# Performance work log

Hardware: AMD Instinct MI355X
Metric: run time of the kernel (lower is better)

The kernel has to match this reference:

```python
import jax, jax.numpy as jnp
import numpy as np

B, S, D, H, DFF, L, VOCAB = 4, 2048, 512, 8, 2048, 6, 32000
DK = D // H


def positional_encoding(n_step, d):
    pos = jnp.arange(n_step, dtype=jnp.float32)[:, None]            # (S,1)
    i = jnp.arange(d, dtype=jnp.float32)                            # (D,)
    ang = pos * (1.0 / jnp.power(10000.0, 2.0 * jnp.floor(i / 2.0) / d))
    odd = (jnp.arange(d) % 2).astype(bool)
    return jnp.where(odd, jnp.cos(ang), jnp.sin(ang))               # (S,D)


def layer_norm(x, g, b, eps=1e-6):
    m = x.mean(-1, keepdims=True)
    v = ((x - m) ** 2).mean(-1, keepdims=True)
    return g * (x - m) * jax.lax.rsqrt(v + eps) + b


def mha(Q, K, V, Wq, bq, Wo, bo, mask):
    # Faithful to source: Wq is (buggily) used for Q, K and V projections.
    def split(t):
        return t.reshape(t.shape[0], -1, H, DK).transpose(0, 2, 1, 3)  # (B,H,S,dk)
    q = split(Q @ Wq + bq)
    k = split(K @ Wq + bq)
    v = split(V @ Wq + bq)
    scores = jnp.einsum('bhqd,bhkd->bhqk', q, k) / jnp.sqrt(jnp.float32(DK))
    if mask is not None:
        scores = scores + mask * (-1e9)
    attn = jax.nn.softmax(scores, axis=-1)
    out = jnp.einsum('bhqk,bhkd->bhqd', attn, v)
    out = out.transpose(0, 2, 1, 3).reshape(Q.shape[0], -1, D)
    return out @ Wo + bo


def setup_inputs() -> dict:
    key = jax.random.key(0)
    ks = jax.random.split(key, 16)
    inputs = jax.random.randint(ks[0], (B, S), 0, VOCAB)
    enc_inputs = jax.random.normal(ks[1], (B, S, D), dtype=jnp.float32)
    # causal mask (1 = masked) broadcast over heads, per source mask*-1e9 convention
    comb = 1.0 - jnp.tril(jnp.ones((S, S), dtype=jnp.float32))
    comb_mask = jnp.broadcast_to(comb, (B, 1, S, S))
    padding_mask = jnp.zeros((B, 1, 1, S), dtype=jnp.float32)
    s = 0.02
    emb = jax.random.normal(ks[2], (VOCAB, D), dtype=jnp.float32) * s
    Wq1 = jax.random.normal(ks[3], (L, D, D), dtype=jnp.float32) * s
    bq1 = jnp.zeros((L, D), dtype=jnp.float32)
    Wo1 = jax.random.normal(ks[4], (L, D, D), dtype=jnp.float32) * s
    bo1 = jnp.zeros((L, D), dtype=jnp.float32)
    Wq2 = jax.random.normal(ks[5], (L, D, D), dtype=jnp.float32) * s
    bq2 = jnp.zeros((L, D), dtype=jnp.float32)
    Wo2 = jax.random.normal(ks[6], (L, D, D), dtype=jnp.float32) * s
    bo2 = jnp.zeros((L, D), dtype=jnp.float32)
    W1 = jax.random.normal(ks[7], (L, D, DFF), dtype=jnp.float32) * s
    b1 = jnp.zeros((L, DFF), dtype=jnp.float32)
    W2 = jax.random.normal(ks[8], (L, DFF, D), dtype=jnp.float32) * s
    b2 = jnp.zeros((L, D), dtype=jnp.float32)
    ln_g = jnp.ones((L, 3, D), dtype=jnp.float32)
    ln_b = jnp.zeros((L, 3, D), dtype=jnp.float32)
    return dict(inputs=inputs, enc_inputs=enc_inputs, comb_mask=comb_mask,
                padding_mask=padding_mask, emb=emb, Wq1=Wq1, bq1=bq1, Wo1=Wo1,
                bo1=bo1, Wq2=Wq2, bq2=bq2, Wo2=Wo2, bo2=bo2, W1=W1, b1=b1,
                W2=W2, b2=b2, ln_g=ln_g, ln_b=ln_b)


def reference(inputs, enc_inputs, comb_mask, padding_mask, emb, Wq1, bq1, Wo1,
              bo1, Wq2, bq2, Wo2, bo2, W1, b1, W2, b2, ln_g, ln_b):
    # embedding + sinusoidal positional encoding (dropout = identity at eval)
    x = emb[inputs] * jnp.sqrt(jnp.float32(D)) + positional_encoding(S, D)
    for l in range(L):
        a1 = mha(x, x, x, Wq1[l], bq1[l], Wo1[l], bo1[l], comb_mask)
        x1 = layer_norm(a1 + x, ln_g[l, 0], ln_b[l, 0])
        a2 = mha(x1, enc_inputs, enc_inputs, Wq2[l], bq2[l], Wo2[l], bo2[l], padding_mask)
        x2 = layer_norm(a2 + x1, ln_g[l, 1], ln_b[l, 1])
        f = jax.nn.relu(x2 @ W1[l] + b1[l]) @ W2[l] + b2[l]
        x = layer_norm(x2 + f, ln_g[l, 2], ln_b[l, 2])
    return x
```

## Files before the change

### kernel.cpp

```cpp
#include <hip/hip_runtime.h>
#include <hip/hip_bf16.h>
#include <cstddef>
#include <cstdint>

#define BB   4
#define SS   2048
#define DD   512
#define HH   8
#define DFFC 2048
#define LLC  6
#define DKH  64
#define MMR  (BB * SS)

typedef short s16x8 __attribute__((ext_vector_type(8)));
typedef short s16x4 __attribute__((ext_vector_type(4)));
typedef float f32x4 __attribute__((ext_vector_type(4)));
typedef unsigned short us4 __attribute__((ext_vector_type(4)));
typedef unsigned int u32;
typedef unsigned int u32x4 __attribute__((ext_vector_type(4)));

__device__ __forceinline__ unsigned short f2bf(float f) {
  union { float f; unsigned int u; } v; v.f = f;
  const unsigned int u = v.u;
  return (unsigned short)((u + 0x7FFFu + ((u >> 16) & 1u)) >> 16);
}
__device__ __forceinline__ float bflo(u32 u) { return __uint_as_float(u << 16); }
__device__ __forceinline__ float bfhi(u32 u) { return __uint_as_float(u & 0xffff0000u); }

__device__ __forceinline__ s16x8 ld8(const unsigned short* p) {
  return *(const s16x8*)p;
}

__device__ __forceinline__ u32 cvtpk(float a, float b) {
  u32 r;
  asm("v_cvt_pk_bf16_f32 %0, %1, %2" : "=v"(r) : "v"(a), "v"(b));
  return r;
}

__device__ __forceinline__ void gload16(const unsigned short* g, unsigned short* l) {
  __builtin_amdgcn_global_load_lds(
      (const __attribute__((address_space(1))) void*)g,
      (__attribute__((address_space(3))) void*)l, 16, 0, 0);
}

__global__ __launch_bounds__(256) void k_embed_pe(const int* __restrict__ toks,
                                                  const float* __restrict__ emb,
                                                  unsigned short* __restrict__ xb) {
  const int t = blockIdx.x;
  const int s = t & (SS - 1);
  const int tok = toks[t];
  const float ln10k = 9.210340371976184f;
  for (int d = threadIdx.x; d < DD; d += 256) {
    const int e = d >> 1;
    const float ex = 2.0f * (float)e * (1.0f / (float)DD);
    const float freq = expf(-ex * ln10k);
    const float ang = (float)s * freq;
    const float pe = (d & 1) ? cosf(ang) : sinf(ang);
    const float v = emb[(size_t)tok * DD + d] * 22.62741699796952f + pe;
    xb[(size_t)t * DD + d] = f2bf(v);
  }
}

__global__ __launch_bounds__(256) void k_f32_to_bf16(const float* __restrict__ src,
                                                     unsigned short* __restrict__ dst) {
  const int i = (blockIdx.x * 256 + threadIdx.x) * 4;
  const float4 v = *(const float4*)(src + i);
  us4 w;
  w.x = f2bf(v.x); w.y = f2bf(v.y); w.z = f2bf(v.z); w.w = f2bf(v.w);
  *(us4*)(dst + i) = w;
}

__global__ __launch_bounds__(256) void k_wt(const float* s0, const float* s1,
                                            const float* s2, const float* s3,
                                            const float* s4, const float* s5,
                                            unsigned short* d0, unsigned short* d1,
                                            unsigned short* d2, unsigned short* d3,
                                            unsigned short* d4, unsigned short* d5) {
  const int t = blockIdx.x;
  const int tid = threadIdx.x;
  const float* src; unsigned short* dst; int K, N, tile, lntn;
  if (t < 256) {
    const int m = t >> 6; tile = t & 63; K = 512; N = 512; lntn = 3;
    src = (m == 0) ? s0 : (m == 1) ? s1 : (m == 2) ? s2 : s3;
    dst = (m == 0) ? d0 : (m == 1) ? d1 : (m == 2) ? d2 : d3;
  } else if (t < 512) {
    src = s4; dst = d4; K = 512; N = 2048; tile = t - 256; lntn = 5;
  } else {
    src = s5; dst = d5; K = 2048; N = 512; tile = t - 512; lntn = 3;
  }
  const int tn = tile & ((1 << lntn) - 1);
  const int tk = tile >> lntn;
  const int k0 = tk * 64, n0 = tn * 64;

  __shared__ unsigned short T[64][68];
#pragma unroll
  for (int i = 0; i < 4; ++i) {
    const int f = i * 256 + tid;
    const int r = f >> 4, c4 = (f & 15) << 2;
    const float4 v = *(const float4*)(src + (size_t)(k0 + r) * N + n0 + c4);
    us4 w;
    w.x = f2bf(v.x); w.y = f2bf(v.y); w.z = f2bf(v.z); w.w = f2bf(v.w);
    *(us4*)&T[r][c4] = w;
  }
  __syncthreads();
#pragma unroll
  for (int i = 0; i < 4; ++i) {
    const int f = i * 256 + tid;
    const int n = f >> 4, k4 = (f & 15) << 2;
    us4 w;
    w.x = T[k4 + 0][n]; w.y = T[k4 + 1][n];
    w.z = T[k4 + 2][n]; w.w = T[k4 + 3][n];
    *(us4*)&dst[(size_t)(n0 + n) * K + k0 + k4] = w;
  }
}

template<int BN, bool RELU, bool VT>
__global__ __launch_bounds__(256) void k_gemm_mfma(const unsigned short* __restrict__ A,
                                                   const unsigned short* __restrict__ Bt,
                                                   const float* __restrict__ bias,
                                                   unsigned short* __restrict__ Cb,
                                                   unsigned short* __restrict__ Vt,
                                                   int voff, int M, int N, int K) {
  constexpr int NT = BN / 32;
  __shared__ unsigned short As[128 * 64];
  __shared__ unsigned short Bs[BN * 64];

  const int tid = threadIdx.x;
  const int wave = tid >> 6, lane = tid & 63;
  const int quad = lane >> 4, l16 = lane & 15;
  const int wm = wave & 1, wn = wave >> 1;
  const int mbase = blockIdx.x * 128, nbase = blockIdx.y * BN;

  f32x4 acc[4][NT];
#pragma unroll
  for (int mt = 0; mt < 4; ++mt)
#pragma unroll
    for (int nt = 0; nt < NT; ++nt) acc[mt][nt] = (f32x4){0.f, 0.f, 0.f, 0.f};

  for (int kb = 0; kb < K; kb += 64) {
    __syncthreads();
#pragma unroll
    for (int i = 0; i < 4; ++i) {
      const int c = i * 256 + wave * 64 + lane;
      const int m = c >> 3;
      const int k8 = (c & 7) ^ (m & 7);
      gload16(A + (size_t)(mbase + m) * K + kb + k8 * 8,
              As + (size_t)(i * 256 + wave * 64) * 8);
    }
#pragma unroll
    for (int i = 0; i < BN / 32; ++i) {
      const int c = i * 256 + wave * 64 + lane;
      const int n = c >> 3;
      const int k8 = (c & 7) ^ (n & 7);
      gload16(Bt + (size_t)(nbase + n) * K + kb + k8 * 8,
              Bs + (size_t)(i * 256 + wave * 64) * 8);
    }
    __syncthreads();
#pragma unroll
    for (int kh = 0; kh < 2; ++kh) {
      s16x8 af[4];
#pragma unroll
      for (int mt = 0; mt < 4; ++mt) {
        const int m = wm * 64 + mt * 16 + l16;
        const int cc = m * 8 + ((kh * 4 + quad) ^ (m & 7));
        af[mt] = ld8(As + cc * 8);
      }
#pragma unroll
      for (int nt = 0; nt < NT; ++nt) {
        const int n = wn * (BN / 2) + nt * 16 + l16;
        const int cc = n * 8 + ((kh * 4 + quad) ^ (n & 7));
        const s16x8 bf = ld8(Bs + cc * 8);
#pragma unroll
        for (int mt = 0; mt < 4; ++mt)
          acc[mt][nt] = __builtin_amdgcn_mfma_f32_16x16x32_bf16(af[mt], bf, acc[mt][nt], 0, 0, 0);
      }
    }
  }

#pragma unroll
  for (int nt = 0; nt < NT; ++nt) {
    const int col = nbase + wn * (BN / 2) + nt * 16 + l16;
    const float bv = bias[col];
#pragma unroll
    for (int mt = 0; mt < 4; ++mt) {
      const int row0 = mbase + wm * 64 + mt * 16 + quad * 4;
      float vv[4];
#pragma unroll
      for (int r = 0; r < 4; ++r) {
        float v = acc[mt][nt][r] + bv;
        if (RELU) v = fmaxf(v, 0.0f);
        vv[r] = v;
        Cb[(size_t)(row0 + r) * N + col] = f2bf(v);
      }
      if (VT) {
        if (row0 >= voff) {
          const int vrow = row0 - voff;
          const int bb = vrow >> 11, s0 = vrow & 2047;
          const int g = (s0 >> 2) & 15;
          const int pos = (g & 8) + ((g & 3) << 1) + ((g >> 2) & 1);
          const int s0p = (s0 & ~63) | (pos << 2);
          us4 o;
          o.x = f2bf(vv[0]); o.y = f2bf(vv[1]); o.z = f2bf(vv[2]); o.w = f2bf(vv[3]);
          *(us4*)(Vt + ((size_t)((bb * 8 + (col >> 6)) * 64 + (col & 63))) * SS + s0p) = o;
        }
      }
    }
  }
}

__global__ __launch_bounds__(512, 4) void k_attn_mfma(const unsigned short* __restrict__ Qp,
                                                      const unsigned short* __restrict__ Kp,
                                                      const unsigned short* __restrict__ Vtp,
                                                      unsigned short* __restrict__ Out,
                                                      int causal) {
  __shared__ __align__(16) unsigned char smem[34816];
  unsigned short* KsB = (unsigned short*)smem;
  unsigned short* VsB = (unsigned short*)(smem + 16384);

  const int hb = blockIdx.x;
  const int h = hb & 7, b = hb >> 3;
  const int by = blockIdx.y;
  const int qt = causal ? ((by < 8) ? (15 - by) : (by - 8)) : by;
  const int tid = threadIdx.x;
  const int w = tid >> 6, lane = tid & 63;
  const int quad = lane >> 4, l16 = lane & 15;
  const int qg = w & 3, ks = w >> 2;

  s16x8 aq[2][2];
#pragma unroll
  for (int mt = 0; mt < 2; ++mt) {
    const int qrow = b * SS + qt * 128 + qg * 32 + mt * 16 + l16;
#pragma unroll
    for (int kh = 0; kh < 2; ++kh) {
      s16x8 v = *(const s16x8*)(Qp + (size_t)qrow * DD + h * DKH + kh * 32 + quad * 8);
#pragma unroll
      for (int j = 0; j < 8; ++j) {
        const unsigned int u = ((unsigned int)(unsigned short)v[j]) << 16;
        const float f = __uint_as_float(u) * 0.125f;
        v[j] = (short)(unsigned short)(__float_as_uint(f) >> 16);
      }
      aq[mt][kh] = v;
    }
  }

  f32x4 O[2][4];
  float l_r[2];
#pragma unroll
  for (int mt = 0; mt < 2; ++mt) {
    l_r[mt] = 0.f;
#pragma unroll
    for (int i = 0; i < 4; ++i) O[mt][i] = (f32x4){0.f, 0.f, 0.f, 0.f};
  }

  const unsigned short* Kb = Kp + (size_t)(b * SS) * DD + h * DKH;
  const unsigned short* Vb = Vtp + (size_t)hb * DKH * SS;

  const int nkt = causal ? (2 * qt + 2) : (SS / 64);

  auto stage = [&](int kt2, int buf) {
    const int r = tid >> 3, c8 = tid & 7;
    gload16(Kb + (size_t)(kt2 * 64 + r) * DD + ((c8 ^ (r & 7)) << 3),
            KsB + buf * 4096 + w * 512);
    gload16(Vb + (size_t)r * SS + kt2 * 64 + ((c8 ^ (r & 7)) << 3),
            VsB + buf * 4096 + w * 512);
  };

  stage(0, 0);
  for (int kt = 0; kt < nkt; ++kt) {
    __syncthreads();
    if (kt + 1 < nkt) stage(kt + 1, (kt + 1) & 1);
    const unsigned short* ksp = KsB + (kt & 1) * 4096;
    const unsigned short* vsp = VsB + (kt & 1) * 4096;

    s16x8 kf[2][2];
#pragma unroll
    for (int kg = 0; kg < 2; ++kg) {
      const int row = ks * 32 + kg * 16 + l16;
#pragma unroll
      for (int kh = 0; kh < 2; ++kh)
        kf[kg][kh] = ld8(ksp + (row * 8 + ((kh * 4 + quad) ^ (row & 7))) * 8);
    }

    f32x4 S[2][2];
    __builtin_amdgcn_s_setprio(1);
#pragma unroll
    for (int mt = 0; mt < 2; ++mt)
#pragma unroll
      for (int kg = 0; kg < 2; ++kg) {
        f32x4 s = (f32x4){0.f, 0.f, 0.f, 0.f};
        s = __builtin_amdgcn_mfma_f32_16x16x32_bf16(kf[kg][0], aq[mt][0], s, 0, 0, 0);
        s = __builtin_amdgcn_mfma_f32_16x16x32_bf16(kf[kg][1], aq[mt][1], s, 0, 0, 0);
        S[mt][kg] = s;
      }
    __builtin_amdgcn_s_setprio(0);

    s16x8 vbf[4];
#pragma unroll
    for (int nt = 0; nt < 4; ++nt) {
      const int d = nt * 16 + l16;
      vbf[nt] = ld8(vsp + (d * 8 + ((ks * 4 + quad) ^ (d & 7))) * 8);
    }

    s16x8 pa[2];
#pragma unroll
    for (int mt = 0; mt < 2; ++mt) {
      const int qb = qt * 128 + qg * 32 + mt * 16;
      const bool needmask = causal && (kt * 64 + 63 > qb);
      const int q = qb + l16;
      float pv[2][4];
#pragma unroll
      for (int kg = 0; kg < 2; ++kg) {
#pragma unroll
        for (int r = 0; r < 4; ++r) {
          float p = __expf(S[mt][kg][r]);
          if (needmask) {
            const int key = kt * 64 + ks * 32 + kg * 16 + quad * 4 + r;
            if (key > q) p = 0.0f;
          }
          pv[kg][r] = p;
        }
      }
      l_r[mt] += ((pv[0][0] + pv[0][1]) + (pv[0][2] + pv[0][3]))
               + ((pv[1][0] + pv[1][1]) + (pv[1][2] + pv[1][3]));
      u32x4 pk;
      pk.x = cvtpk(pv[0][0], pv[0][1]);
      pk.y = cvtpk(pv[0][2], pv[0][3]);
      pk.z = cvtpk(pv[1][0], pv[1][1]);
      pk.w = cvtpk(pv[1][2], pv[1][3]);
      pa[mt] = __builtin_bit_cast(s16x8, pk);
    }

    __builtin_amdgcn_s_setprio(1);
#pragma unroll
    for (int nt = 0; nt < 4; ++nt)
#pragma unroll
      for (int mt = 0; mt < 2; ++mt)
        O[mt][nt] = __builtin_amdgcn_mfma_f32_16x16x32_bf16(pa[mt], vbf[nt], O[mt][nt], 0, 0, 0);
    __builtin_amdgcn_s_setprio(0);
  }

  float lq[2][4];
#pragma unroll
  for (int mt = 0; mt < 2; ++mt) {
    float l = l_r[mt];
    l += __shfl_xor(l, 16);
    l += __shfl_xor(l, 32);
#pragma unroll
    for (int r = 0; r < 4; ++r)
      lq[mt][r] = __shfl(l, quad * 4 + r);
  }

  __syncthreads();
  float* Obuf = (float*)smem;
  float* Lbuf = (float*)(smem + 33792);
  if (ks == 1) {
#pragma unroll
    for (int mt = 0; mt < 2; ++mt)
#pragma unroll
      for (int r = 0; r < 4; ++r) {
        const int row = qg * 32 + mt * 16 + quad * 4 + r;
        if (l16 == 0) Lbuf[row] = lq[mt][r];
#pragma unroll
        for (int nt = 0; nt < 4; ++nt)
          Obuf[(size_t)row * 66 + nt * 16 + l16] = O[mt][nt][r];
      }
  }
  __syncthreads();
  if (ks == 0) {
#pragma unroll
    for (int mt = 0; mt < 2; ++mt)
#pragma unroll
      for (int r = 0; r < 4; ++r) {
        const int row = qg * 32 + mt * 16 + quad * 4 + r;
        const float linv = 1.0f / (lq[mt][r] + Lbuf[row]);
        unsigned short* orow = Out + (size_t)(b * SS + qt * 128 + row) * DD + h * DKH;
#pragma unroll
        for (int nt = 0; nt < 4; ++nt)
          orow[nt * 16 + l16] = f2bf((O[mt][nt][r] + Obuf[(size_t)row * 66 + nt * 16 + l16]) * linv);
      }
  }
}

__device__ __forceinline__ float block_reduce_sum(float v) {
  __shared__ float red[4];
#pragma unroll
  for (int off = 32; off > 0; off >>= 1) v += __shfl_down(v, off);
  const int lane = threadIdx.x & 63;
  const int w = threadIdx.x >> 6;
  __syncthreads();
  if (lane == 0) red[w] = v;
  __syncthreads();
  return red[0] + red[1] + red[2] + red[3];
}

template<bool F32OUT>
__global__ __launch_bounds__(256) void k_add_ln(const unsigned short* __restrict__ a,
                                                const unsigned short* __restrict__ r,
                                                const float* __restrict__ g,
                                                const float* __restrict__ be,
                                                unsigned short* __restrict__ ob,
                                                float* __restrict__ of) {
  const int row = blockIdx.x;
  const int t = threadIdx.x;
  const size_t base = (size_t)row * DD + t * 2;
  const u32 av = *(const u32*)(a + base);
  const u32 rv = *(const u32*)(r + base);
  const float v0 = bflo(av) + bflo(rv);
  const float v1 = bfhi(av) + bfhi(rv);
  const float s = block_reduce_sum(v0 + v1);
  const float mean = s * (1.0f / (float)DD);
  const float d0 = v0 - mean;
  const float d1 = v1 - mean;
  const float var = block_reduce_sum(d0 * d0 + d1 * d1) * (1.0f / (float)DD);
  const float inv = rsqrtf(var + 1e-6f);
  const float o0 = g[t * 2] * d0 * inv + be[t * 2];
  const float o1 = g[t * 2 + 1] * d1 * inv + be[t * 2 + 1];
  const u32 o = (u32)f2bf(o0) | ((u32)f2bf(o1) << 16);
  *(u32*)(ob + base) = o;
  if (F32OUT) {
    of[base]     = o0;
    of[base + 1] = o1;
  }
}

extern "C" void kernel_launch(void* const* d_in, const int* in_sizes, int n_in,
                              void* d_out, int out_size, void* d_ws, size_t ws_size,
                              hipStream_t stream) {
  const int*   toks = (const int*)d_in[0];
  const float* enc  = (const float*)d_in[1];
  const float* emb  = (const float*)d_in[4];
  const float* Wq1  = (const float*)d_in[5];
  const float* bq1  = (const float*)d_in[6];
  const float* Wo1  = (const float*)d_in[7];
  const float* bo1  = (const float*)d_in[8];
  const float* Wq2  = (const float*)d_in[9];
  const float* bq2  = (const float*)d_in[10];
  const float* Wo2  = (const float*)d_in[11];
  const float* bo2  = (const float*)d_in[12];
  const float* W1   = (const float*)d_in[13];
  const float* b1   = (const float*)d_in[14];
  const float* W2   = (const float*)d_in[15];
  const float* b2   = (const float*)d_in[16];
  const float* lng  = (const float*)d_in[17];
  const float* lnb  = (const float*)d_in[18];
  float* out = (float*)d_out;

  char* p = (char*)d_ws;
  unsigned short* Wq1t = (unsigned short*)p; p += (size_t)512 * 512 * 2;
  unsigned short* Wo1t = (unsigned short*)p; p += (size_t)512 * 512 * 2;
  unsigned short* Wq2t = (unsigned short*)p; p += (size_t)512 * 512 * 2;
  unsigned short* Wo2t = (unsigned short*)p; p += (size_t)512 * 512 * 2;
  unsigned short* W1t  = (unsigned short*)p; p += (size_t)2048 * 512 * 2;
  unsigned short* W2t  = (unsigned short*)p; p += (size_t)512 * 2048 * 2;
  unsigned short* Xcur = (unsigned short*)p; p += (size_t)MMR * DD * 2;
  unsigned short* Cat  = (unsigned short*)p; p += (size_t)2 * MMR * DD * 2;
  unsigned short* Pm   = (unsigned short*)p; p += (size_t)2 * MMR * DD * 2;
  unsigned short* Ab   = (unsigned short*)p; p += (size_t)MMR * DD * 2;
  unsigned short* Gb   = (unsigned short*)p; p += (size_t)MMR * DD * 2;
  unsigned short* X2b  = (unsigned short*)p; p += (size_t)MMR * DD * 2;
  unsigned short* Vt   = (unsigned short*)p; p += (size_t)MMR * DD * 2;
  unsigned short* Hb   = (unsigned short*)p; p += (size_t)MMR * DFFC * 2;
  unsigned short* encb = Cat + (size_t)MMR * DD;

  const dim3 blk(256);
  const dim3 blkA(512);
  const dim3 gP(MMR / 128, DD / 64);
  const dim3 gM(2 * MMR / 128, DD / 64);
  const dim3 gF1(MMR / 128, DFFC / 128);
  const dim3 gAttn(HH * BB, SS / 128);

  k_embed_pe<<<MMR, blk, 0, stream>>>(toks, emb, Xcur);
  k_f32_to_bf16<<<(MMR * DD) / 1024, blk, 0, stream>>>(enc, encb);

  for (int l = 0; l < LLC; ++l) {
    const float* wq1 = Wq1 + (size_t)l * DD * DD;
    const float* wo1 = Wo1 + (size_t)l * DD * DD;
    const float* wq2 = Wq2 + (size_t)l * DD * DD;
    const float* wo2 = Wo2 + (size_t)l * DD * DD;
    const float* w1  = W1  + (size_t)l * DD * DFFC;
    const float* w2  = W2  + (size_t)l * DFFC * DD;
    const float* bq1l = bq1 + (size_t)l * DD;
    const float* bo1l = bo1 + (size_t)l * DD;
    const float* bq2l = bq2 + (size_t)l * DD;
    const float* bo2l = bo2 + (size_t)l * DD;
    const float* b1l  = b1  + (size_t)l * DFFC;
    const float* b2l  = b2  + (size_t)l * DD;
    const float* g0 = lng + ((size_t)l * 3 + 0) * DD;
    const float* e0 = lnb + ((size_t)l * 3 + 0) * DD;
    const float* g1 = lng + ((size_t)l * 3 + 1) * DD;
    const float* e1 = lnb + ((size_t)l * 3 + 1) * DD;
    const float* g2 = lng + ((size_t)l * 3 + 2) * DD;
    const float* e2 = lnb + ((size_t)l * 3 + 2) * DD;

    k_wt<<<768, blk, 0, stream>>>(wq1, wo1, wq2, wo2, w1, w2,
                                  Wq1t, Wo1t, Wq2t, Wo2t, W1t, W2t);

    k_gemm_mfma<64, false, true><<<gP, blk, 0, stream>>>(Xcur, Wq1t, bq1l, Pm, Vt, 0, MMR, DD, DD);
    k_attn_mfma<<<gAttn, blkA, 0, stream>>>(Pm, Pm, Vt, Ab, 1);
    k_gemm_mfma<64, false, false><<<gP, blk, 0, stream>>>(Ab, Wo1t, bo1l, Gb, nullptr, 0, MMR, DD, DD);
    k_add_ln<false><<<MMR, blk, 0, stream>>>(Gb, Xcur, g0, e0, Cat, nullptr);

    k_gemm_mfma<64, false, true><<<gM, blk, 0, stream>>>(Cat, Wq2t, bq2l, Pm, Vt, MMR, 2 * MMR, DD, DD);
    k_attn_mfma<<<gAttn, blkA, 0, stream>>>(Pm, Pm + (size_t)MMR * DD, Vt, Ab, 0);
    k_gemm_mfma<64, false, false><<<gP, blk, 0, stream>>>(Ab, Wo2t, bo2l, Gb, nullptr, 0, MMR, DD, DD);
    k_add_ln<false><<<MMR, blk, 0, stream>>>(Gb, Cat, g1, e1, X2b, nullptr);

    k_gemm_mfma<128, true, false><<<gF1, blk, 0, stream>>>(X2b, W1t, b1l, Hb, nullptr, 0, MMR, DFFC, DD);
    k_gemm_mfma<64, false, false><<<gP, blk, 0, stream>>>(Hb, W2t, b2l, Gb, nullptr, 0, MMR, DD, DFFC);
    if (l == LLC - 1)
      k_add_ln<true><<<MMR, blk, 0, stream>>>(Gb, X2b, g2, e2, Xcur, out);
    else
      k_add_ln<false><<<MMR, blk, 0, stream>>>(Gb, X2b, g2, e2, Xcur, nullptr);
  }
}
```

Baseline: 1.532 ms.

## Double-buffer GEMM shared tiles and use one wave per row in add+layernorm

The GEMM kernel now keeps two shared-memory buffers for the A and B tiles and issues the next K-tile's async loads before computing on the current one. This overlaps global-to-LDS traffic with MFMA work, at the cost of twice the LDS per block and possibly lower occupancy. The add+layernorm kernel is rewritten so each 64-lane wave handles one row with 16-byte vector loads and stores and wave shuffle reductions. This removes the block-level reductions and their __syncthreads. The LN launch grid changes to four rows per block.

```diff
diff --git a/kernel.cpp b/kernel.cpp
--- a/kernel.cpp
+++ b/kernel.cpp
@@ -122,8 +122,8 @@
                                                    unsigned short* __restrict__ Vt,
                                                    int voff, int M, int N, int K) {
   constexpr int NT = BN / 32;
-  __shared__ unsigned short As[128 * 64];
-  __shared__ unsigned short Bs[BN * 64];
+  __shared__ unsigned short As[2][128 * 64];
+  __shared__ unsigned short Bs[2][BN * 64];
 
   const int tid = threadIdx.x;
   const int wave = tid >> 6, lane = tid & 63;
@@ -137,25 +137,32 @@
 #pragma unroll
     for (int nt = 0; nt < NT; ++nt) acc[mt][nt] = (f32x4){0.f, 0.f, 0.f, 0.f};
 
-  for (int kb = 0; kb < K; kb += 64) {
-    __syncthreads();
+  auto stage = [&](int kb, int buf) {
 #pragma unroll
     for (int i = 0; i < 4; ++i) {
       const int c = i * 256 + wave * 64 + lane;
       const int m = c >> 3;
       const int k8 = (c & 7) ^ (m & 7);
-      gload16(A + (size_t)(mbase + m) * K + kb + k8 * 8,
-              As + (size_t)(i * 256 + wave * 64) * 8);
+      gload16(A + (size_t)(mbase + m) * K + kb * 64 + k8 * 8,
+              As[buf] + (size_t)(i * 256 + wave * 64) * 8);
     }
 #pragma unroll
     for (int i = 0; i < BN / 32; ++i) {
       const int c = i * 256 + wave * 64 + lane;
       const int n = c >> 3;
       const int k8 = (c & 7) ^ (n & 7);
-      gload16(Bt + (size_t)(nbase + n) * K + kb + k8 * 8,
-              Bs + (size_t)(i * 256 + wave * 64) * 8);
-    }
+      gload16(Bt + (size_t)(nbase + n) * K + kb * 64 + k8 * 8,
+              Bs[buf] + (size_t)(i * 256 + wave * 64) * 8);
+    }
+  };
+
+  const int nkb = K / 64;
+  stage(0, 0);
+  for (int kb = 0; kb < nkb; ++kb) {
     __syncthreads();
+    if (kb + 1 < nkb) stage(kb + 1, (kb + 1) & 1);
+    const unsigned short* as = As[kb & 1];
+    const unsigned short* bs = Bs[kb & 1];
 #pragma unroll
     for (int kh = 0; kh < 2; ++kh) {
       s16x8 af[4];
@@ -163,13 +170,13 @@
       for (int mt = 0; mt < 4; ++mt) {
         const int m = wm * 64 + mt * 16 + l16;
         const int cc = m * 8 + ((kh * 4 + quad) ^ (m & 7));
-        af[mt] = ld8(As + cc * 8);
+        af[mt] = ld8(as + cc * 8);
       }
 #pragma unroll
       for (int nt = 0; nt < NT; ++nt) {
         const int n = wn * (BN / 2) + nt * 16 + l16;
         const int cc = n * 8 + ((kh * 4 + quad) ^ (n & 7));
-        const s16x8 bf = ld8(Bs + cc * 8);
+        const s16x8 bf = ld8(bs + cc * 8);
 #pragma unroll
         for (int mt = 0; mt < 4; ++mt)
           acc[mt][nt] = __builtin_amdgcn_mfma_f32_16x16x32_bf16(af[mt], bf, acc[mt][nt], 0, 0, 0);
@@ -381,18 +388,6 @@
   }
 }
 
-__device__ __forceinline__ float block_reduce_sum(float v) {
-  __shared__ float red[4];
-#pragma unroll
-  for (int off = 32; off > 0; off >>= 1) v += __shfl_down(v, off);
-  const int lane = threadIdx.x & 63;
-  const int w = threadIdx.x >> 6;
-  __syncthreads();
-  if (lane == 0) red[w] = v;
-  __syncthreads();
-  return red[0] + red[1] + red[2] + red[3];
-}
-
 template<bool F32OUT>
 __global__ __launch_bounds__(256) void k_add_ln(const unsigned short* __restrict__ a,
                                                 const unsigned short* __restrict__ r,
@@ -400,26 +395,50 @@
                                                 const float* __restrict__ be,
                                                 unsigned short* __restrict__ ob,
                                                 float* __restrict__ of) {
-  const int row = blockIdx.x;
-  const int t = threadIdx.x;
-  const size_t base = (size_t)row * DD + t * 2;
-  const u32 av = *(const u32*)(a + base);
-  const u32 rv = *(const u32*)(r + base);
-  const float v0 = bflo(av) + bflo(rv);
-  const float v1 = bfhi(av) + bfhi(rv);
-  const float s = block_reduce_sum(v0 + v1);
+  const int row = blockIdx.x * 4 + (threadIdx.x >> 6);
+  const int lane = threadIdx.x & 63;
+  const size_t base = (size_t)row * DD + lane * 8;
+  const u32x4 av = *(const u32x4*)(a + base);
+  const u32x4 rv = *(const u32x4*)(r + base);
+  float v[8];
+  float s = 0.f;
+#pragma unroll
+  for (int i = 0; i < 4; ++i) {
+    const float lo = bflo(av[i]) + bflo(rv[i]);
+    const float hi = bfhi(av[i]) + bfhi(rv[i]);
+    v[2 * i] = lo; v[2 * i + 1] = hi;
+    s += lo + hi;
+  }
+#pragma unroll
+  for (int off = 32; off > 0; off >>= 1) s += __shfl_xor(s, off);
   const float mean = s * (1.0f / (float)DD);
-  const float d0 = v0 - mean;
-  const float d1 = v1 - mean;
-  const float var = block_reduce_sum(d0 * d0 + d1 * d1) * (1.0f / (float)DD);
-  const float inv = rsqrtf(var + 1e-6f);
-  const float o0 = g[t * 2] * d0 * inv + be[t * 2];
-  const float o1 = g[t * 2 + 1] * d1 * inv + be[t * 2 + 1];
-  const u32 o = (u32)f2bf(o0) | ((u32)f2bf(o1) << 16);
-  *(u32*)(ob + base) = o;
+  float vs = 0.f;
+#pragma unroll
+  for (int i = 0; i < 8; ++i) { v[i] -= mean; vs += v[i] * v[i]; }
+#pragma unroll
+  for (int off = 32; off > 0; off >>= 1) vs += __shfl_xor(vs, off);
+  const float inv = rsqrtf(vs * (1.0f / (float)DD) + 1e-6f);
+  const float4 g0 = *(const float4*)(g + lane * 8);
+  const float4 g1 = *(const float4*)(g + lane * 8 + 4);
+  const float4 b0 = *(const float4*)(be + lane * 8);
+  const float4 b1 = *(const float4*)(be + lane * 8 + 4);
+  float o[8];
+  o[0] = g0.x * v[0] * inv + b0.x;
+  o[1] = g0.y * v[1] * inv + b0.y;
+  o[2] = g0.z * v[2] * inv + b0.z;
+  o[3] = g0.w * v[3] * inv + b0.w;
+  o[4] = g1.x * v[4] * inv + b1.x;
+  o[5] = g1.y * v[5] * inv + b1.y;
+  o[6] = g1.z * v[6] * inv + b1.z;
+  o[7] = g1.w * v[7] * inv + b1.w;
+  u32x4 w;
+#pragma unroll
+  for (int i = 0; i < 4; ++i)
+    w[i] = (u32)f2bf(o[2 * i]) | ((u32)f2bf(o[2 * i + 1]) << 16);
+  *(u32x4*)(ob + base) = w;
   if (F32OUT) {
-    of[base]     = o0;
-    of[base + 1] = o1;
+    *(float4*)(of + base)     = (float4){o[0], o[1], o[2], o[3]};
+    *(float4*)(of + base + 4) = (float4){o[4], o[5], o[6], o[7]};
   }
 }
 
@@ -468,6 +487,7 @@
   const dim3 gM(2 * MMR / 128, DD / 64);
   const dim3 gF1(MMR / 128, DFFC / 128);
   const dim3 gAttn(HH * BB, SS / 128);
+  const dim3 gLN(MMR / 4);
 
   k_embed_pe<<<MMR, blk, 0, stream>>>(toks, emb, Xcur);
   k_f32_to_bf16<<<(MMR * DD) / 1024, blk, 0, stream>>>(enc, encb);
@@ -498,18 +518,18 @@
     k_gemm_mfma<64, false, true><<<gP, blk, 0, stream>>>(Xcur, Wq1t, bq1l, Pm, Vt, 0, MMR, DD, DD);
     k_attn_mfma<<<gAttn, blkA, 0, stream>>>(Pm, Pm, Vt, Ab, 1);
     k_gemm_mfma<64, false, false><<<gP, blk, 0, stream>>>(Ab, Wo1t, bo1l, Gb, nullptr, 0, MMR, DD, DD);
-    k_add_ln<false><<<MMR, blk, 0, stream>>>(Gb, Xcur, g0, e0, Cat, nullptr);
+    k_add_ln<false><<<gLN, blk, 0, stream>>>(Gb, Xcur, g0, e0, Cat, nullptr);
 
     k_gemm_mfma<64, false, true><<<gM, blk, 0, stream>>>(Cat, Wq2t, bq2l, Pm, Vt, MMR, 2 * MMR, DD, DD);
     k_attn_mfma<<<gAttn, blkA, 0, stream>>>(Pm, Pm + (size_t)MMR * DD, Vt, Ab, 0);
     k_gemm_mfma<64, false, false><<<gP, blk, 0, stream>>>(Ab, Wo2t, bo2l, Gb, nullptr, 0, MMR, DD, DD);
-    k_add_ln<false><<<MMR, blk, 0, stream>>>(Gb, Cat, g1, e1, X2b, nullptr);
+    k_add_ln<false><<<gLN, blk, 0, stream>>>(Gb, Cat, g1, e1, X2b, nullptr);
 
     k_gemm_mfma<128, true, false><<<gF1, blk, 0, stream>>>(X2b, W1t, b1l, Hb, nullptr, 0, MMR, DFFC, DD);
     k_gemm_mfma<64, false, false><<<gP, blk, 0, stream>>>(Hb, W2t, b2l, Gb, nullptr, 0, MMR, DD, DFFC);
     if (l == LLC - 1)
-      k_add_ln<true><<<MMR, blk, 0, stream>>>(Gb, X2b, g2, e2, Xcur, out);
+      k_add_ln<true><<<gLN, blk, 0, stream>>>(Gb, X2b, g2, e2, Xcur, out);
     else
-      k_add_ln<false><<<MMR, blk, 0, stream>>>(Gb, X2b, g2, e2, Xcur, nullptr);
-  }
-}
+      k_add_ln<false><<<gLN, blk, 0, stream>>>(Gb, X2b, g2, e2, Xcur, nullptr);
+  }
+}
```

New measurement: 1.437 ms. 1.07x faster.
